# Kernel tuning notes

Measured on AMD Instinct MI355X. Metric: run time of the kernel, lower is better.

Reference implementation:

```python
import jax, jax.numpy as jnp
import numpy as np

EPS = 1e-7  # tf.keras.backend.epsilon()
NEG_RATIO = 3.0
MIN_NEG = 10000

B, H, W = 32, 384, 384


def setup_inputs() -> dict:
    key = jax.random.key(0)
    ks = jax.random.split(key, 6)
    shape = (B, H, W)
    region_true = jax.random.uniform(ks[0], shape, dtype=jnp.float32)
    affinity_true = jax.random.uniform(ks[1], shape, dtype=jnp.float32)
    region_pred = jax.random.uniform(ks[2], shape, dtype=jnp.float32)
    affinity_pred = jax.random.uniform(ks[3], shape, dtype=jnp.float32)
    confidence = jax.random.uniform(ks[4], shape, dtype=jnp.float32)
    u = jax.random.uniform(ks[5], shape, dtype=jnp.float32)
    fg_mask = (u < 0.3).astype(jnp.float32)
    bg_mask = (u >= 0.3).astype(jnp.float32)
    return {
        "region_true": region_true,
        "affinity_true": affinity_true,
        "region_pred": region_pred,
        "affinity_pred": affinity_pred,
        "confidence": confidence,
        "fg_mask": fg_mask,
        "bg_mask": bg_mask,
    }


def _ohem(loss, fg_mask, bg_mask):
    # per-sample hard-negative mining: keep the top neg_num background losses
    fg_num = jnp.sum(fg_mask)
    bg_num = jnp.sum(bg_mask)
    neg_num = jnp.maximum((fg_num * NEG_RATIO).astype(jnp.int32),
                          jnp.int32(MIN_NEG))
    neg_num = jnp.minimum(bg_num.astype(jnp.int32), neg_num)
    neg_loss = loss * bg_mask                       # [H, W]
    flat = neg_loss.reshape(-1)                     # [H*W]
    sorted_desc = jnp.sort(flat)[::-1]              # descending (== tf.nn.top_k values)
    thresh = sorted_desc[neg_num - 1]               # k-th largest bg loss
    hard = jnp.logical_and(bg_mask.astype(bool), neg_loss >= thresh)
    return hard.astype(jnp.float32)


def _craft_mse_loss(region_true, affinity_true, region_pred, affinity_pred,
                    confidence, fg_mask, bg_mask):
    l_region = jnp.square(region_true - region_pred) * confidence
    l_affinity = jnp.square(affinity_true - affinity_pred) * confidence
    l_total = l_region + l_affinity                 # [B, H, W]
    hard_bg_mask = jax.vmap(_ohem)(l_total, fg_mask, bg_mask)
    train_mask = hard_bg_mask + fg_mask
    num = jnp.sum(l_total * train_mask)
    den = jnp.sum(confidence * train_mask) + EPS
    return num / den


def reference(region_true, affinity_true, region_pred, affinity_pred,
              confidence, fg_mask, bg_mask):
    return _craft_mse_loss(region_true, affinity_true, region_pred,
                           affinity_pred, confidence, fg_mask, bg_mask)
```

## Files before the change

### kernel.cpp

```cpp
#include <hip/hip_runtime.h>

#define HW (384 * 384)
#define BATCH 32
#define HW4 (HW / 4)
#define K1_BLOCKS 144
#define ITER 2
#define K3_BLOCKS 72

#define S_FG 0
#define S_BG 32
#define S_NUMF 64
#define S_DENF 96
#define S_THR 128
#define S_FLAG 160
#define S_GNUM 192
#define S_GDEN 193

__device__ __forceinline__ void fadd_agent(float* p, float v) {
    __hip_atomic_fetch_add(p, v, __ATOMIC_RELAXED, __HIP_MEMORY_SCOPE_AGENT);
}

__device__ __forceinline__ void wave_reduce4(float& a, float& b, float& c, float& d) {
#pragma unroll
    for (int off = 32; off; off >>= 1) {
        a += __shfl_xor(a, off);
        b += __shfl_xor(b, off);
        c += __shfl_xor(c, off);
        d += __shfl_xor(d, off);
    }
}

__global__ __launch_bounds__(256) void k1_stats(
        const float* __restrict__ rt, const float* __restrict__ at,
        const float* __restrict__ rp, const float* __restrict__ ap,
        const float* __restrict__ cf, const float* __restrict__ fg,
        const float* __restrict__ bg, float* __restrict__ stats) {
    __shared__ float lds[4 * 7 * 256];
    const int wave = threadIdx.x >> 6;
    const int lane = threadIdx.x & 63;
    const int b = blockIdx.y;
    const long gi = ((long)b * HW4 + blockIdx.x * 256 + threadIdx.x) * 4;
    float* lb = &lds[wave * (7 * 256)];

#define STAGE(q, arr) __builtin_amdgcn_global_load_lds(                        \
        (const __attribute__((address_space(1))) void*)((arr) + gi),           \
        (__attribute__((address_space(3))) void*)(lb + (q) * 256), 16, 0, 0)
    STAGE(0, rt); STAGE(1, at); STAGE(2, rp); STAGE(3, ap);
    STAGE(4, cf); STAGE(5, fg); STAGE(6, bg);
#undef STAGE
    __syncthreads();

    const float4 vrt = *(const float4*)&lb[0 * 256 + lane * 4];
    const float4 vat = *(const float4*)&lb[1 * 256 + lane * 4];
    const float4 vrp = *(const float4*)&lb[2 * 256 + lane * 4];
    const float4 vap = *(const float4*)&lb[3 * 256 + lane * 4];
    const float4 vcf = *(const float4*)&lb[4 * 256 + lane * 4];
    const float4 vfg = *(const float4*)&lb[5 * 256 + lane * 4];
    const float4 vbg = *(const float4*)&lb[6 * 256 + lane * 4];

    float sfg = 0.f, sbg = 0.f, snum = 0.f, sden = 0.f;
#pragma unroll
    for (int j = 0; j < 4; ++j) {
        float r = (&vrt.x)[j] - (&vrp.x)[j];
        float a = (&vat.x)[j] - (&vap.x)[j];
        float c = (&vcf.x)[j];
        float lt = (r * r + a * a) * c;
        float f = (&vfg.x)[j], g = (&vbg.x)[j];
        float train = f + g;
        sfg += f; sbg += g; snum += lt * train; sden += c * train;
    }

    wave_reduce4(sfg, sbg, snum, sden);
    __shared__ float sh[4][4];
    if (lane == 0) {
        sh[wave][0] = sfg; sh[wave][1] = sbg; sh[wave][2] = snum; sh[wave][3] = sden;
    }
    __syncthreads();
    if (threadIdx.x < 4) {
        const int q = threadIdx.x;
        float s = sh[0][q] + sh[1][q] + sh[2][q] + sh[3][q];
        fadd_agent(&stats[q * 32 + b], s);
    }
}

__global__ __launch_bounds__(512) void k2_select(
        const float* __restrict__ rt, const float* __restrict__ at,
        const float* __restrict__ rp, const float* __restrict__ ap,
        const float* __restrict__ cf, const float* __restrict__ bg,
        float* __restrict__ stats) {
    const int b = blockIdx.x;
    const float fg_num = stats[S_FG + b];
    const float bg_num = stats[S_BG + b];
    int neg = (int)(fg_num * 3.0f);
    if (neg < 10000) neg = 10000;
    const int bgn = (int)bg_num;
    unsigned* flags = (unsigned*)stats;
    if (neg >= bgn) {
        if (threadIdx.x == 0) {
            flags[S_FLAG + b] = 1u;
            fadd_agent(&stats[S_GNUM], stats[S_NUMF + b]);
            fadd_agent(&stats[S_GDEN], stats[S_DENF + b]);
        }
        return;
    }
    if (threadIdx.x == 0) flags[S_FLAG + b] = 0u;

    __shared__ unsigned hist[256];
    __shared__ unsigned sh_prefix, sh_k;
    unsigned prefix = 0;
    unsigned k = (unsigned)neg;
    const long base = (long)b * HW;
#pragma unroll 1
    for (int p = 3; p >= 0; --p) {
        for (int i = threadIdx.x; i < 256; i += blockDim.x) hist[i] = 0u;
        __syncthreads();
        const unsigned shift = 8u * (unsigned)p;
        const unsigned himask = (p == 3) ? 0u : (0xFFFFFFFFu << (shift + 8u));
#pragma unroll 1
        for (int i = threadIdx.x; i < HW; i += blockDim.x) {
            long g = base + i;
            float r = rt[g] - rp[g];
            float a = at[g] - ap[g];
            float lt = (r * r + a * a) * cf[g];
            float nl = lt * bg[g];
            unsigned v = __float_as_uint(nl);
            if ((v & himask) == prefix) atomicAdd(&hist[(v >> shift) & 255u], 1u);
        }
        __syncthreads();
        if (threadIdx.x == 0) {
            unsigned cum = 0;
            for (int bin = 255; bin >= 0; --bin) {
                unsigned c = hist[bin];
                if (cum + c >= k) {
                    sh_prefix = prefix | ((unsigned)bin << shift);
                    sh_k = k - cum;
                    break;
                }
                cum += c;
            }
        }
        __syncthreads();
        prefix = sh_prefix;
        k = sh_k;
        __syncthreads();
    }
    if (threadIdx.x == 0) stats[S_THR + b] = __uint_as_float(prefix);
}

__global__ __launch_bounds__(256) void k3_general(
        const float4* __restrict__ rt, const float4* __restrict__ at,
        const float4* __restrict__ rp, const float4* __restrict__ ap,
        const float4* __restrict__ cf, const float4* __restrict__ fg,
        const float4* __restrict__ bg, float* __restrict__ stats) {
    const int b = blockIdx.y;
    if (((const unsigned*)stats)[S_FLAG + b] != 0u) return;
    const float thresh = stats[S_THR + b];
    const int base = b * HW4 + blockIdx.x * (256 * ITER) + threadIdx.x;
    float snum = 0.f, sden = 0.f, z0 = 0.f, z1 = 0.f;
#pragma unroll
    for (int it = 0; it < ITER; ++it) {
        const int idx = base + it * 256;
        float4 vrt = rt[idx], vat = at[idx], vrp = rp[idx], vap = ap[idx];
        float4 vcf = cf[idx], vfg = fg[idx], vbg = bg[idx];
#pragma unroll
        for (int j = 0; j < 4; ++j) {
            float r = (&vrt.x)[j] - (&vrp.x)[j];
            float a = (&vat.x)[j] - (&vap.x)[j];
            float c = (&vcf.x)[j];
            float lt = (r * r + a * a) * c;
            float f = (&vfg.x)[j], g = (&vbg.x)[j];
            float nl = lt * g;
            float hard = (g != 0.f && nl >= thresh) ? 1.f : 0.f;
            float train = hard + f;
            snum += lt * train;
            sden += c * train;
        }
    }
    wave_reduce4(snum, sden, z0, z1);
    __shared__ float sh[4][2];
    const int wave = threadIdx.x >> 6;
    if ((threadIdx.x & 63) == 0) { sh[wave][0] = snum; sh[wave][1] = sden; }
    __syncthreads();
    if (threadIdx.x < 2) {
        const int q = threadIdx.x;
        float s = sh[0][q] + sh[1][q] + sh[2][q] + sh[3][q];
        fadd_agent(&stats[S_GNUM + q], s);
    }
}

__global__ void k4_final(const float* __restrict__ stats, float* __restrict__ out) {
    out[0] = stats[S_GNUM] / (stats[S_GDEN] + 1e-7f);
}

extern "C" void kernel_launch(void* const* d_in, const int* in_sizes, int n_in,
                              void* d_out, int out_size, void* d_ws, size_t ws_size,
                              hipStream_t stream) {
    const float* rt = (const float*)d_in[0];
    const float* at = (const float*)d_in[1];
    const float* rp = (const float*)d_in[2];
    const float* ap = (const float*)d_in[3];
    const float* cf = (const float*)d_in[4];
    const float* fg = (const float*)d_in[5];
    const float* bg = (const float*)d_in[6];
    float* stats = (float*)d_ws;
    float* out = (float*)d_out;

    hipMemsetAsync(d_ws, 0, 1024, stream);

    dim3 grid1(K1_BLOCKS, BATCH);
    k1_stats<<<grid1, 256, 0, stream>>>(rt, at, rp, ap, cf, fg, bg, stats);
    k2_select<<<BATCH, 512, 0, stream>>>(rt, at, rp, ap, cf, bg, stats);
    dim3 grid3(K3_BLOCKS, BATCH);
    k3_general<<<grid3, 256, 0, stream>>>((const float4*)rt, (const float4*)at,
                                          (const float4*)rp, (const float4*)ap,
                                          (const float4*)cf, (const float4*)fg,
                                          (const float4*)bg, stats);
    k4_final<<<1, 1, 0, stream>>>(stats, out);
}
```

Before: 188.1 us.

## Make stats kernel persistent per wave with double-buffered async LDS staging

The first statistics kernel changes from one 256-float4 tile per block to a fixed 512-block grid. Each wave now streams nine consecutive chunks of its sample through a double-buffered LDS ring, issuing the next chunk's global-to-LDS loads before it computes the current one, with explicit vmcnt/lgkmcnt waits. This is meant to hide memory latency and cut launch and block overhead on what is likely the dominant bandwidth-bound pass. Per-wave atomics replace the block-level LDS reduction, which adds more global atomics, and the hand-placed waits and inline-asm LDS reads add fragility.

```diff
diff --git a/kernel.cpp b/kernel.cpp
--- a/kernel.cpp
+++ b/kernel.cpp
@@ -3,9 +3,14 @@
 #define HW (384 * 384)
 #define BATCH 32
 #define HW4 (HW / 4)
-#define K1_BLOCKS 144
+#define TOTAL_F4 (BATCH * HW4)
+#define K1_GRID 512
+#define F4_PER_WAVE (TOTAL_F4 / 2048)
+#define CHUNKS 9
+#define WAVES_PER_SAMPLE 64
 #define ITER 2
 #define K3_BLOCKS 72
+
 
 #define S_FG 0
 #define S_BG 32
@@ -16,6 +21,9 @@
 #define S_GNUM 192
 #define S_GDEN 193
 
+typedef __attribute__((address_space(3))) float lds_f;
+typedef __attribute__((address_space(1))) const void gv;
+
 __device__ __forceinline__ void fadd_agent(float* p, float v) {
     __hip_atomic_fetch_add(p, v, __ATOMIC_RELAXED, __HIP_MEMORY_SCOPE_AGENT);
 }
@@ -30,56 +38,83 @@
     }
 }
 
+__device__ __forceinline__ float4 lds_read16(unsigned byteaddr) {
+    float4 r;
+    asm volatile("ds_read_b128 %0, %1" : "=v"(r) : "v"(byteaddr));
+    return r;
+}
+#define WAITVM(n) do { asm volatile("s_waitcnt vmcnt(" #n ")" ::: "memory");  \
+                       __builtin_amdgcn_sched_barrier(0); } while (0)
+#define WAITLGKM() do { asm volatile("s_waitcnt lgkmcnt(0)" ::: "memory");    \
+                        __builtin_amdgcn_sched_barrier(0); } while (0)
+
 __global__ __launch_bounds__(256) void k1_stats(
         const float* __restrict__ rt, const float* __restrict__ at,
         const float* __restrict__ rp, const float* __restrict__ ap,
         const float* __restrict__ cf, const float* __restrict__ fg,
         const float* __restrict__ bg, float* __restrict__ stats) {
-    __shared__ float lds[4 * 7 * 256];
+    __shared__ float lds[4 * 2 * 7 * 256];
     const int wave = threadIdx.x >> 6;
     const int lane = threadIdx.x & 63;
-    const int b = blockIdx.y;
-    const long gi = ((long)b * HW4 + blockIdx.x * 256 + threadIdx.x) * 4;
-    float* lb = &lds[wave * (7 * 256)];
-
-#define STAGE(q, arr) __builtin_amdgcn_global_load_lds(                        \
-        (const __attribute__((address_space(1))) void*)((arr) + gi),           \
-        (__attribute__((address_space(3))) void*)(lb + (q) * 256), 16, 0, 0)
-    STAGE(0, rt); STAGE(1, at); STAGE(2, rp); STAGE(3, ap);
-    STAGE(4, cf); STAGE(5, fg); STAGE(6, bg);
+    const int w = blockIdx.x * 4 + wave;
+    const int b = w >> 6;
+    const long f4w = (long)w * F4_PER_WAVE;
+
+    lds_f* lwave = (lds_f*)&lds[wave * (2 * 7 * 256)];
+    const unsigned lbase = (unsigned)(uintptr_t)lwave;
+
+#define STAGE(buf, c) do {                                                     \
+        const long _g = (f4w + (long)(c) * 64 + lane) * 4;                     \
+        lds_f* _d = lwave + (buf) * (7 * 256);                                 \
+        __builtin_amdgcn_global_load_lds((gv*)(rt + _g), (lds_f*)(_d + 0*256), 16, 0, 0); \
+        __builtin_amdgcn_global_load_lds((gv*)(at + _g), (lds_f*)(_d + 1*256), 16, 0, 0); \
+        __builtin_amdgcn_global_load_lds((gv*)(rp + _g), (lds_f*)(_d + 2*256), 16, 0, 0); \
+        __builtin_amdgcn_global_load_lds((gv*)(ap + _g), (lds_f*)(_d + 3*256), 16, 0, 0); \
+        __builtin_amdgcn_global_load_lds((gv*)(cf + _g), (lds_f*)(_d + 4*256), 16, 0, 0); \
+        __builtin_amdgcn_global_load_lds((gv*)(fg + _g), (lds_f*)(_d + 5*256), 16, 0, 0); \
+        __builtin_amdgcn_global_load_lds((gv*)(bg + _g), (lds_f*)(_d + 6*256), 16, 0, 0); \
+    } while (0)
+
+    float sfg = 0.f, sbg = 0.f, snum = 0.f, sden = 0.f;
+
+    STAGE(0, 0);
+#pragma unroll
+    for (int c = 0; c < CHUNKS; ++c) {
+        const int cur = c & 1;
+        if (c + 1 < CHUNKS) {
+            STAGE(cur ^ 1, c + 1);
+            WAITVM(7);
+        } else {
+            WAITVM(0);
+        }
+        const unsigned rb = lbase + cur * (7 * 1024) + lane * 16;
+        float4 vrt = lds_read16(rb + 0 * 1024);
+        float4 vat = lds_read16(rb + 1 * 1024);
+        float4 vrp = lds_read16(rb + 2 * 1024);
+        float4 vap = lds_read16(rb + 3 * 1024);
+        float4 vcf = lds_read16(rb + 4 * 1024);
+        float4 vfg = lds_read16(rb + 5 * 1024);
+        float4 vbg = lds_read16(rb + 6 * 1024);
+        WAITLGKM();
+#pragma unroll
+        for (int j = 0; j < 4; ++j) {
+            float r = (&vrt.x)[j] - (&vrp.x)[j];
+            float a = (&vat.x)[j] - (&vap.x)[j];
+            float cc = (&vcf.x)[j];
+            float lt = (r * r + a * a) * cc;
+            float f = (&vfg.x)[j], g = (&vbg.x)[j];
+            float train = f + g;
+            sfg += f; sbg += g; snum += lt * train; sden += cc * train;
+        }
+    }
 #undef STAGE
-    __syncthreads();
-
-    const float4 vrt = *(const float4*)&lb[0 * 256 + lane * 4];
-    const float4 vat = *(const float4*)&lb[1 * 256 + lane * 4];
-    const float4 vrp = *(const float4*)&lb[2 * 256 + lane * 4];
-    const float4 vap = *(const float4*)&lb[3 * 256 + lane * 4];
-    const float4 vcf = *(const float4*)&lb[4 * 256 + lane * 4];
-    const float4 vfg = *(const float4*)&lb[5 * 256 + lane * 4];
-    const float4 vbg = *(const float4*)&lb[6 * 256 + lane * 4];
-
-    float sfg = 0.f, sbg = 0.f, snum = 0.f, sden = 0.f;
-#pragma unroll
-    for (int j = 0; j < 4; ++j) {
-        float r = (&vrt.x)[j] - (&vrp.x)[j];
-        float a = (&vat.x)[j] - (&vap.x)[j];
-        float c = (&vcf.x)[j];
-        float lt = (r * r + a * a) * c;
-        float f = (&vfg.x)[j], g = (&vbg.x)[j];
-        float train = f + g;
-        sfg += f; sbg += g; snum += lt * train; sden += c * train;
-    }
 
     wave_reduce4(sfg, sbg, snum, sden);
-    __shared__ float sh[4][4];
     if (lane == 0) {
-        sh[wave][0] = sfg; sh[wave][1] = sbg; sh[wave][2] = snum; sh[wave][3] = sden;
-    }
-    __syncthreads();
-    if (threadIdx.x < 4) {
-        const int q = threadIdx.x;
-        float s = sh[0][q] + sh[1][q] + sh[2][q] + sh[3][q];
-        fadd_agent(&stats[q * 32 + b], s);
+        fadd_agent(&stats[S_FG + b], sfg);
+        fadd_agent(&stats[S_BG + b], sbg);
+        fadd_agent(&stats[S_NUMF + b], snum);
+        fadd_agent(&stats[S_DENF + b], sden);
     }
 }
 
@@ -207,8 +242,7 @@
 
     hipMemsetAsync(d_ws, 0, 1024, stream);
 
-    dim3 grid1(K1_BLOCKS, BATCH);
-    k1_stats<<<grid1, 256, 0, stream>>>(rt, at, rp, ap, cf, fg, bg, stats);
+    k1_stats<<<K1_GRID, 256, 0, stream>>>(rt, at, rp, ap, cf, fg, bg, stats);
     k2_select<<<BATCH, 512, 0, stream>>>(rt, at, rp, ap, cf, bg, stats);
     dim3 grid3(K3_BLOCKS, BATCH);
     k3_general<<<grid3, 256, 0, stream>>>((const float4*)rt, (const float4*)at,
```

Measured after the change: 176.0 us. 6.4% less time.
